# Performance work log

Measured on AMD Instinct MI355X. Metric: run time of the kernel, lower is better.

The kernel has to match this reference:

```python
import jax, jax.numpy as jnp
import numpy as np

BS, T = 128, 256
N_AGENTS, N_ATOM = 8, 51
V_MIN, V_MAX = -10.0, 10.0
STATE_DIM = 120


def setup_inputs() -> dict:
    key = jax.random.key(0)
    k1, k2 = jax.random.split(key)
    p = jax.random.uniform(k1, (BS, T, N_AGENTS, N_ATOM), dtype=jnp.float32)
    p = p / p.sum(-1, keepdims=True)  # per-agent PMFs
    states = jax.random.normal(k2, (BS, T, STATE_DIM), dtype=jnp.float32)
    return {"agent_qs_distri": p, "states": states}


def _bconv(a, b):
    """Batched full convolution of two PMFs along the last axis.
    a: [..., La], b: [..., Lb] -> [..., La+Lb-1]."""
    lead = a.shape[:-1]
    a2 = a.reshape(-1, a.shape[-1])
    b2 = b.reshape(-1, b.shape[-1])
    out = jax.vmap(lambda x, y: jnp.convolve(x, y, mode="full"))(a2, b2)
    return out.reshape(*lead, -1)


def _proj(supports, probs, v_min, v_max, n_atom):
    """C51 categorical projection onto n_atom atoms in [v_min, v_max].
    supports/probs: [..., K] -> [..., n_atom] via floor/ceil scatter-add."""
    delta = (v_max - v_min) / (n_atom - 1)
    b = (jnp.clip(supports, v_min, v_max) - v_min) / delta  # fractional bin
    l = jnp.floor(b)
    wl = l + 1.0 - b  # mass to lower atom (all mass when b is integral)
    wu = b - l        # mass to upper atom
    li = l.astype(jnp.int32)
    K = probs.shape[-1]
    flat_p = probs.reshape(-1, K)
    flat_l = li.reshape(-1, K)
    flat_wl = wl.reshape(-1, K)
    flat_wu = wu.reshape(-1, K)
    rows = jnp.arange(flat_p.shape[0], dtype=jnp.int32)[:, None]
    idx_l = rows * n_atom + jnp.clip(flat_l, 0, n_atom - 1)
    idx_u = rows * n_atom + jnp.clip(flat_l + 1, 0, n_atom - 1)
    out = jnp.zeros(flat_p.shape[0] * n_atom, dtype=probs.dtype)
    out = out.at[idx_l.ravel()].add((flat_p * flat_wl).ravel())
    out = out.at[idx_u.ravel()].add((flat_p * flat_wu).ravel())
    return out.reshape(*probs.shape[:-1], n_atom)


def reference(agent_qs_distri, states):
    # sequential PMF convolution over agents (support grows each step)
    q_tot = agent_qs_distri[:, :, 0]
    for i in range(1, N_AGENTS):
        q_tot = _bconv(q_tot, agent_qs_distri[:, :, i])
    # q_tot: [BS, T, N_AGENTS*N_ATOM - N_AGENTS + 1]
    support = jnp.linspace(N_AGENTS * V_MIN, N_AGENTS * V_MAX,
                           N_AGENTS * N_ATOM - N_AGENTS + 1, dtype=jnp.float32)
    support = jnp.broadcast_to(support, q_tot.shape)
    return _proj(support, q_tot, V_MIN, V_MAX, N_ATOM)
```

## Files before the change

kernel.cpp:

```cpp
#include <hip/hip_runtime.h>


#define N_ATOM  51
#define N_TASKS 32768
#define BUFSZ   512
#define PAD     50
#define WPB     4

template<int R>
__device__ __forceinline__ void conv_step(const float* __restrict__ gp,
                                          const float* bin, float* bout, int lane) {
  float pv = (lane < N_ATOM) ? gp[lane] : 0.f;
  const int o0 = lane * R;
  float W[R + PAD];
#pragma unroll
  for (int w = 0; w < R + PAD; ++w) W[w] = bin[o0 + w];
  float acc[R];
#pragma unroll
  for (int r = 0; r < R; ++r) acc[r] = 0.f;
#pragma unroll
  for (int j = 0; j < N_ATOM; ++j) {
    float pj = __builtin_bit_cast(float,
        __builtin_amdgcn_readlane(__builtin_bit_cast(int, pv), j));
#pragma unroll
    for (int r = 0; r < R; ++r)
      acc[r] = fmaf(pj, W[r - j + PAD], acc[r]);
  }
#pragma unroll
  for (int r = 0; r < R; ++r) bout[PAD + o0 + r] = acc[r];
}

__global__ __launch_bounds__(256, 4)
void dvdn_mixer_kernel(const float* __restrict__ in, float* __restrict__ out) {
  __shared__ float buf[WPB][2][BUFSZ];
  const int lane = threadIdx.x & 63;
  const int wave = threadIdx.x >> 6;
  const int task = blockIdx.x * WPB + wave;

  const float* gp = in + (size_t)task * (8 * N_ATOM);
  float* b0 = buf[wave][0];
  float* b1 = buf[wave][1];

#pragma unroll
  for (int i = lane; i < BUFSZ; i += 64) { b0[i] = 0.f; b1[i] = 0.f; }
  if (lane < N_ATOM) b0[PAD + lane] = gp[lane];
  __syncthreads();

  conv_step<3>(gp + 1 * N_ATOM, b0, b1, lane); __syncthreads();
  conv_step<3>(gp + 2 * N_ATOM, b1, b0, lane); __syncthreads();
  conv_step<5>(gp + 3 * N_ATOM, b0, b1, lane); __syncthreads();
  conv_step<5>(gp + 4 * N_ATOM, b1, b0, lane); __syncthreads();
  conv_step<5>(gp + 5 * N_ATOM, b0, b1, lane); __syncthreads();
  conv_step<7>(gp + 6 * N_ATOM, b1, b0, lane); __syncthreads();
  conv_step<7>(gp + 7 * N_ATOM, b0, b1, lane); __syncthreads();

  const float* q = b1 + PAD;

  float s0 = 0.f, s1 = 0.f;
  for (int k = lane; k < 176; k += 64)       s0 += q[k];
  for (int k = 225 + lane; k < 401; k += 64) s1 += q[k];
#pragma unroll
  for (int d = 1; d < 64; d <<= 1) {
    s0 += __shfl_xor(s0, d, 64);
    s1 += __shfl_xor(s1, d, 64);
  }

  float* o = out + (size_t)task * N_ATOM;
  if (lane == 0) { o[0] = s0; o[50] = s1; }
  else if (lane < 50) o[lane] = q[175 + lane];
}

extern "C" void kernel_launch(void* const* d_in, const int* in_sizes, int n_in,
                              void* d_out, int out_size, void* d_ws, size_t ws_size,
                              hipStream_t stream) {
  const float* agent_qs = (const float*)d_in[0];
  float* out = (float*)d_out;
  dvdn_mixer_kernel<<<N_TASKS / WPB, 256, 0, stream>>>(agent_qs, out);
}
```

Before: 216.8 us.

## Vectorize LDS traffic, use uniform scalar PMF loads, fuse final conv with projection

Outputs per lane become multiples of four (4 then 8), so LDS windows are read and written as float4, with padding widened to keep 16-byte alignment. The task index is forced wave-uniform so each agent's PMF is read through scalar loads into registers instead of 51 per-step readlane broadcasts. The last convolution step keeps its results in registers and feeds the edge sums and direct output stores, skipping the final LDS write and reread. Per-lane work grows in some steps and the occupancy hint in launch_bounds is removed, so register pressure and wasted FMAs on padded outputs may increase.

```diff
diff --git a/kernel.cpp b/kernel.cpp
--- a/kernel.cpp
+++ b/kernel.cpp
@@ -3,71 +3,104 @@
 
 #define N_ATOM  51
 #define N_TASKS 32768
-#define BUFSZ   512
-#define PAD     50
 #define WPB     4
+#define PAD     52
+#define BUFSZ   576
+
+template<int R>
+__device__ __forceinline__ void conv_body(const float* __restrict__ gp,
+                                          const float* bin, float* acc, int lane) {
+  constexpr int NW = (R + PAD + 3) / 4;
+  const int o0 = lane * R;
+  float W[NW * 4];
+  const float4* src = reinterpret_cast<const float4*>(bin + o0);
+#pragma unroll
+  for (int w = 0; w < NW; ++w) {
+    float4 v = src[w];
+    W[4 * w + 0] = v.x; W[4 * w + 1] = v.y;
+    W[4 * w + 2] = v.z; W[4 * w + 3] = v.w;
+  }
+  float p[N_ATOM];
+#pragma unroll
+  for (int j = 0; j < N_ATOM; ++j) p[j] = gp[j];
+#pragma unroll
+  for (int r = 0; r < R; ++r) acc[r] = 0.f;
+#pragma unroll
+  for (int j = 0; j < N_ATOM; ++j)
+#pragma unroll
+    for (int r = 0; r < R; ++r)
+      acc[r] = fmaf(p[j], W[PAD + r - j], acc[r]);
+}
 
 template<int R>
 __device__ __forceinline__ void conv_step(const float* __restrict__ gp,
                                           const float* bin, float* bout, int lane) {
-  float pv = (lane < N_ATOM) ? gp[lane] : 0.f;
-  const int o0 = lane * R;
-  float W[R + PAD];
+  float acc[R];
+  conv_body<R>(gp, bin, acc, lane);
+  float4* dst = reinterpret_cast<float4*>(bout + PAD + lane * R);
 #pragma unroll
-  for (int w = 0; w < R + PAD; ++w) W[w] = bin[o0 + w];
-  float acc[R];
-#pragma unroll
-  for (int r = 0; r < R; ++r) acc[r] = 0.f;
-#pragma unroll
-  for (int j = 0; j < N_ATOM; ++j) {
-    float pj = __builtin_bit_cast(float,
-        __builtin_amdgcn_readlane(__builtin_bit_cast(int, pv), j));
-#pragma unroll
-    for (int r = 0; r < R; ++r)
-      acc[r] = fmaf(pj, W[r - j + PAD], acc[r]);
-  }
-#pragma unroll
-  for (int r = 0; r < R; ++r) bout[PAD + o0 + r] = acc[r];
+  for (int r4 = 0; r4 < R / 4; ++r4)
+    dst[r4] = make_float4(acc[4 * r4], acc[4 * r4 + 1],
+                          acc[4 * r4 + 2], acc[4 * r4 + 3]);
 }
 
-__global__ __launch_bounds__(256, 4)
+__global__ __launch_bounds__(256)
 void dvdn_mixer_kernel(const float* __restrict__ in, float* __restrict__ out) {
-  __shared__ float buf[WPB][2][BUFSZ];
+  __shared__ __align__(16) float buf[WPB][2][BUFSZ];
   const int lane = threadIdx.x & 63;
   const int wave = threadIdx.x >> 6;
-  const int task = blockIdx.x * WPB + wave;
+  const int task = __builtin_amdgcn_readfirstlane(blockIdx.x * WPB + wave);
 
   const float* gp = in + (size_t)task * (8 * N_ATOM);
   float* b0 = buf[wave][0];
   float* b1 = buf[wave][1];
 
+  {
+    float4* z0 = reinterpret_cast<float4*>(b0);
 #pragma unroll
-  for (int i = lane; i < BUFSZ; i += 64) { b0[i] = 0.f; b1[i] = 0.f; }
-  if (lane < N_ATOM) b0[PAD + lane] = gp[lane];
+    for (int k = lane; k < BUFSZ / 4; k += 64) {
+      const int f = 4 * k - PAD;
+      float4 v = make_float4(0.f, 0.f, 0.f, 0.f);
+      if (f >= 0 && f + 3 < N_ATOM) {
+        v.x = gp[f]; v.y = gp[f + 1]; v.z = gp[f + 2]; v.w = gp[f + 3];
+      } else if (f + 3 >= 0 && f < N_ATOM) {
+        if (f >= 0)         v.x = gp[f];
+        if (f + 1 >= 0 && f + 1 < N_ATOM) v.y = gp[f + 1];
+        if (f + 2 >= 0 && f + 2 < N_ATOM) v.z = gp[f + 2];
+        if (f + 3 < N_ATOM) v.w = gp[f + 3];
+      }
+      z0[k] = v;
+    }
+    float4* z1 = reinterpret_cast<float4*>(b1);
+    if (lane < PAD / 4) z1[lane] = make_float4(0.f, 0.f, 0.f, 0.f);
+  }
   __syncthreads();
 
-  conv_step<3>(gp + 1 * N_ATOM, b0, b1, lane); __syncthreads();
-  conv_step<3>(gp + 2 * N_ATOM, b1, b0, lane); __syncthreads();
-  conv_step<5>(gp + 3 * N_ATOM, b0, b1, lane); __syncthreads();
-  conv_step<5>(gp + 4 * N_ATOM, b1, b0, lane); __syncthreads();
-  conv_step<5>(gp + 5 * N_ATOM, b0, b1, lane); __syncthreads();
-  conv_step<7>(gp + 6 * N_ATOM, b1, b0, lane); __syncthreads();
-  conv_step<7>(gp + 7 * N_ATOM, b0, b1, lane); __syncthreads();
+  conv_step<4>(gp + 1 * N_ATOM, b0, b1, lane); __syncthreads();
+  conv_step<4>(gp + 2 * N_ATOM, b1, b0, lane); __syncthreads();
+  conv_step<4>(gp + 3 * N_ATOM, b0, b1, lane); __syncthreads();
+  conv_step<4>(gp + 4 * N_ATOM, b1, b0, lane); __syncthreads();
+  conv_step<8>(gp + 5 * N_ATOM, b0, b1, lane); __syncthreads();
+  conv_step<8>(gp + 6 * N_ATOM, b1, b0, lane); __syncthreads();
 
-  const float* q = b1 + PAD;
+  float acc[8];
+  conv_body<8>(gp + 7 * N_ATOM, b0, acc, lane);
 
   float s0 = 0.f, s1 = 0.f;
-  for (int k = lane; k < 176; k += 64)       s0 += q[k];
-  for (int k = 225 + lane; k < 401; k += 64) s1 += q[k];
+  float* o = out + (size_t)task * N_ATOM;
+#pragma unroll
+  for (int r = 0; r < 8; ++r) {
+    const int oidx = 8 * lane + r;
+    if (oidx >= 176 && oidx < 225) o[oidx - 175] = acc[r];
+    s0 += (oidx < 176) ? acc[r] : 0.f;
+    s1 += (oidx >= 225) ? acc[r] : 0.f;
+  }
 #pragma unroll
   for (int d = 1; d < 64; d <<= 1) {
     s0 += __shfl_xor(s0, d, 64);
     s1 += __shfl_xor(s1, d, 64);
   }
-
-  float* o = out + (size_t)task * N_ATOM;
   if (lane == 0) { o[0] = s0; o[50] = s1; }
-  else if (lane < 50) o[lane] = q[175 + lane];
 }
 
 extern "C" void kernel_launch(void* const* d_in, const int* in_sizes, int n_in,
```

New measurement: 319.3 us. +47.3%, slower.
